# Kernel tuning notes

Measured on AMD Instinct MI355X. Metric: run time of the kernel, lower is better.

Reference implementation:

```python
import jax, jax.numpy as jnp
import numpy as np

N_NODES = 50000
N_EDGES = 400000
IN_DIM = 256
EPS_BN = 1e-5


def _bn(x, gamma, beta):
    # BatchNorm over nodes (training-mode batch statistics)
    m = jnp.mean(x, axis=0)
    v = jnp.var(x, axis=0)
    return (x - m) * jax.lax.rsqrt(v + EPS_BN) * gamma + beta


def _gcn(x, W, b, src, dst, n):
    # PyG GCNConv: add self-loops, symmetric deg^-1/2 normalization
    h = x @ W  # [N, F_out]
    deg = jax.ops.segment_sum(jnp.ones_like(dst, dtype=h.dtype), dst, num_segments=n) + 1.0
    dinv = jax.lax.rsqrt(deg)
    coef = dinv[src] * dinv[dst]  # [E]
    agg = jax.ops.segment_sum(h[src] * coef[:, None], dst, num_segments=n)
    agg = agg + h * (dinv * dinv)[:, None]  # self-loop contribution
    return agg + b


def _gat(x, W, a_src, a_dst, b, src, dst, n):
    # PyG GATConv, heads=H, concat=False (mean over heads)
    H, F = a_src.shape
    h = (x @ W).reshape(n, H, F)
    asc = jnp.einsum('nhf,hf->nh', h, a_src)
    adc = jnp.einsum('nhf,hf->nh', h, a_dst)
    loops = jnp.arange(n, dtype=src.dtype)
    s = jnp.concatenate([src, loops])
    d = jnp.concatenate([dst, loops])
    e = jax.nn.leaky_relu(asc[s] + adc[d], 0.2)  # [E+N, H]
    mx = jax.ops.segment_max(e, d, num_segments=n)
    ee = jnp.exp(e - mx[d])
    denom = jax.ops.segment_sum(ee, d, num_segments=n)
    alpha = ee / (denom[d] + 1e-16)  # edge softmax over incoming edges
    out = jax.ops.segment_sum(alpha[:, :, None] * h[s], d, num_segments=n)  # [N,H,F]
    return out.mean(axis=1) + b


def setup_inputs() -> dict:
    key = jax.random.key(0)
    ks = jax.random.split(key, 24)

    def glorot(k, shape):
        fan = shape[0] + shape[-1]
        return jax.random.normal(k, shape, jnp.float32) * np.sqrt(2.0 / fan)

    d = {}
    d['x'] = jax.random.normal(ks[0], (N_NODES, IN_DIM), jnp.float32)
    d['edge_index'] = jax.random.randint(ks[1], (2, N_EDGES), 0, N_NODES, jnp.int32)
    # GCNConv 1: 256 -> 256
    d['w1'] = glorot(ks[2], (IN_DIM, 256)); d['b1'] = jnp.zeros((256,), jnp.float32)
    d['g1'] = jnp.ones((256,), jnp.float32); d['be1'] = jnp.zeros((256,), jnp.float32)
    # GATConv: 256 -> 128, heads=4, concat=False
    d['gat_w'] = glorot(ks[3], (256, 4 * 128))
    d['gat_as'] = glorot(ks[4], (4, 128))
    d['gat_ad'] = glorot(ks[5], (4, 128))
    d['gat_b'] = jnp.zeros((128,), jnp.float32)
    d['g2'] = jnp.ones((128,), jnp.float32); d['be2'] = jnp.zeros((128,), jnp.float32)
    # GCNConv 3..5
    d['w3'] = glorot(ks[6], (128, 64)); d['b3'] = jnp.zeros((64,), jnp.float32)
    d['g3'] = jnp.ones((64,), jnp.float32); d['be3'] = jnp.zeros((64,), jnp.float32)
    d['w4'] = glorot(ks[7], (64, 32)); d['b4'] = jnp.zeros((32,), jnp.float32)
    d['g4'] = jnp.ones((32,), jnp.float32); d['be4'] = jnp.zeros((32,), jnp.float32)
    d['w5'] = glorot(ks[8], (32, 16)); d['b5'] = jnp.zeros((16,), jnp.float32)
    d['g5'] = jnp.ones((16,), jnp.float32); d['be5'] = jnp.zeros((16,), jnp.float32)
    # FC head
    d['fw1'] = glorot(ks[9], (16, 8)); d['fb1'] = jnp.zeros((8,), jnp.float32)
    d['fw2'] = glorot(ks[10], (8, 3)); d['fb2'] = jnp.zeros((3,), jnp.float32)
    return d


def reference(x, edge_index, w1, b1, g1, be1, gat_w, gat_as, gat_ad, gat_b, g2, be2,
              w3, b3, g3, be3, w4, b4, g4, be4, w5, b5, g5, be5, fw1, fb1, fw2, fb2):
    n = x.shape[0]
    src, dst = edge_index[0], edge_index[1]
    lrelu = lambda h: jax.nn.leaky_relu(h, 0.01)
    # dropout is identity in eval mode
    h = lrelu(_bn(_gcn(x, w1, b1, src, dst, n), g1, be1))
    h = lrelu(_bn(_gat(h, gat_w, gat_as, gat_ad, gat_b, src, dst, n), g2, be2))
    h = lrelu(_bn(_gcn(h, w3, b3, src, dst, n), g3, be3))
    h = lrelu(_bn(_gcn(h, w4, b4, src, dst, n), g4, be4))
    h = lrelu(_bn(_gcn(h, w5, b5, src, dst, n), g5, be5))
    h = lrelu(h @ fw1 + fb1)
    h = h @ fw2 + fb2
    return jax.nn.log_softmax(h, axis=1)
```

## Files before the change

kernel.cpp:

```cpp
#include <hip/hip_runtime.h>

#define NN 50000
#define NE 400000
#define GSTAT 2048

typedef short bf16x8 __attribute__((ext_vector_type(8)));
typedef float f32x4 __attribute__((ext_vector_type(4)));

__device__ __forceinline__ float lrelu01(float v) { return v >= 0.f ? v : 0.01f * v; }
__device__ __forceinline__ float lrelu02(float v) { return v >= 0.f ? v : 0.2f * v; }

__device__ __forceinline__ ushort f2bf(float f) {
  union { float f; unsigned u; } v; v.f = f;
  unsigned u = v.u;
  return (ushort)((u + 0x7FFFu + ((u >> 16) & 1u)) >> 16);
}
__device__ __forceinline__ float bf2f(ushort u) {
  union { unsigned u; float f; } v; v.u = ((unsigned)u) << 16;
  return v.f;
}

__global__ void wprep(const float* __restrict__ w1, const float* __restrict__ gw,
                      const float* __restrict__ w3, const float* __restrict__ w4,
                      const float* __restrict__ w5,
                      ushort* __restrict__ w1T, ushort* __restrict__ gwT,
                      ushort* __restrict__ w3T, ushort* __restrict__ w4T,
                      ushort* __restrict__ w5T) {
  int i = blockIdx.x * 256 + threadIdx.x;
  const float* W; ushort* WT; int K, N, j;
  if (i < 65536)        { W = w1; WT = w1T; K = 256; N = 256; j = i; }
  else if (i < 196608)  { W = gw; WT = gwT; K = 256; N = 512; j = i - 65536; }
  else if (i < 204800)  { W = w3; WT = w3T; K = 128; N = 64;  j = i - 196608; }
  else if (i < 206848)  { W = w4; WT = w4T; K = 64;  N = 32;  j = i - 204800; }
  else if (i < 207360)  { W = w5; WT = w5T; K = 32;  N = 16;  j = i - 206848; }
  else return;
  int k = j / N, c = j % N;
  WT[(size_t)c * K + k] = f2bf(W[(size_t)j]);
}

__global__ void count_kernel(const int* __restrict__ dst, int* __restrict__ counts, int e) {
  int i = blockIdx.x * 256 + threadIdx.x;
  if (i < e) atomicAdd(&counts[dst[i]], 1);
}

__global__ __launch_bounds__(256) void block_count_sum(const int* __restrict__ counts,
                                                       int* __restrict__ bsum,
                                                       float* __restrict__ dinv, int n) {
  int i = blockIdx.x * 256 + threadIdx.x;
  int c = (i < n) ? counts[i] : 0;
  if (i < n) dinv[i] = rsqrtf((float)c + 1.0f);
  int s = c;
#pragma unroll
  for (int off = 32; off > 0; off >>= 1) s += __shfl_down(s, off);
  __shared__ int ws[4];
  if ((threadIdx.x & 63) == 0) ws[threadIdx.x >> 6] = s;
  __syncthreads();
  if (threadIdx.x == 0) bsum[blockIdx.x] = ws[0] + ws[1] + ws[2] + ws[3];
}

__global__ __launch_bounds__(256) void scan_bsum(int* __restrict__ bsum, int nb) {
  __shared__ int sh[256];
  int v = (threadIdx.x < nb) ? bsum[threadIdx.x] : 0;
  sh[threadIdx.x] = v;
  __syncthreads();
  for (int off = 1; off < 256; off <<= 1) {
    int t = (threadIdx.x >= off) ? sh[threadIdx.x - off] : 0;
    __syncthreads();
    sh[threadIdx.x] += t;
    __syncthreads();
  }
  if (threadIdx.x < nb) bsum[threadIdx.x] = sh[threadIdx.x] - v;
}

__global__ __launch_bounds__(256) void row_start_kernel(const int* __restrict__ counts,
                                                        const int* __restrict__ bsum,
                                                        int* __restrict__ row_start, int n) {
  __shared__ int sh[256];
  int i = blockIdx.x * 256 + threadIdx.x;
  int c = (i < n) ? counts[i] : 0;
  sh[threadIdx.x] = c;
  __syncthreads();
  for (int off = 1; off < 256; off <<= 1) {
    int t = (threadIdx.x >= off) ? sh[threadIdx.x - off] : 0;
    __syncthreads();
    sh[threadIdx.x] += t;
    __syncthreads();
  }
  int incl = sh[threadIdx.x];
  int base = bsum[blockIdx.x];
  if (i < n) row_start[i] = base + incl - c;
  if (i == n - 1) row_start[n] = base + incl;
}

__global__ void fill_kernel(const int* __restrict__ src, const int* __restrict__ dst,
                            const int* __restrict__ row_start, int* __restrict__ cursor,
                            int* __restrict__ csr, int e) {
  int i = blockIdx.x * 256 + threadIdx.x;
  if (i >= e) return;
  int d = dst[i];
  int pos = atomicAdd(&cursor[d], 1);
  csr[row_start[d] + pos] = src[i];
}

__global__ __launch_bounds__(256) void gemm_mfma_x(const float* __restrict__ A,
                                                   const ushort* __restrict__ BT,
                                                   ushort* __restrict__ C,
                                                   int M, int K, int N,
                                                   const float* __restrict__ rowscale) {
  __shared__ ushort As[128][40];
  __shared__ ushort Bs[128][40];
  const int tid = threadIdx.x;
  const int bm = blockIdx.x * 128;
  const int bn = blockIdx.y * 128;
  const int wave = tid >> 6, lane = tid & 63;
  const int wr = (wave >> 1) * 64;
  const int wc = (wave & 1) * 64;
  const int lr = lane & 15;
  const int lk = (lane >> 4) * 8;

  f32x4 acc[4][4];
#pragma unroll
  for (int m = 0; m < 4; ++m)
#pragma unroll
    for (int n = 0; n < 4; ++n)
#pragma unroll
      for (int q = 0; q < 4; ++q) acc[m][n][q] = 0.f;

  for (int k0 = 0; k0 < K; k0 += 32) {
#pragma unroll
    for (int it = 0; it < 2; ++it) {
      int s = tid + it * 256;
      int r = s >> 2;
      int c = (s & 3) * 8;
      int grow = bm + r; if (grow >= M) grow = M - 1;
      float4 va = *reinterpret_cast<const float4*>(&A[(size_t)grow * K + k0 + c]);
      float4 vb = *reinterpret_cast<const float4*>(&A[(size_t)grow * K + k0 + c + 4]);
      ushort4 lo = make_ushort4(f2bf(va.x), f2bf(va.y), f2bf(va.z), f2bf(va.w));
      ushort4 hi = make_ushort4(f2bf(vb.x), f2bf(vb.y), f2bf(vb.z), f2bf(vb.w));
      *reinterpret_cast<ushort4*>(&As[r][c]) = lo;
      *reinterpret_cast<ushort4*>(&As[r][c + 4]) = hi;
    }
#pragma unroll
    for (int it = 0; it < 2; ++it) {
      int s = tid + it * 256;
      int r = s >> 2;
      int c = (s & 3) * 8;
      int4 v = *reinterpret_cast<const int4*>(&BT[(size_t)(bn + r) * K + k0 + c]);
      *reinterpret_cast<int4*>(&Bs[r][c]) = v;
    }
    __syncthreads();

    bf16x8 af[4], bfr[4];
#pragma unroll
    for (int m = 0; m < 4; ++m)
      af[m] = *reinterpret_cast<const bf16x8*>(&As[wr + m * 16 + lr][lk]);
#pragma unroll
    for (int n = 0; n < 4; ++n)
      bfr[n] = *reinterpret_cast<const bf16x8*>(&Bs[wc + n * 16 + lr][lk]);
#pragma unroll
    for (int m = 0; m < 4; ++m)
#pragma unroll
      for (int n = 0; n < 4; ++n)
        acc[m][n] = __builtin_amdgcn_mfma_f32_16x16x32_bf16(af[m], bfr[n], acc[m][n], 0, 0, 0);
    __syncthreads();
  }

  const int rbase = (lane >> 4) * 4;
  const int cbase = lane & 15;
#pragma unroll
  for (int m = 0; m < 4; ++m) {
#pragma unroll
    for (int q = 0; q < 4; ++q) {
      int row = bm + wr + m * 16 + rbase + q;
      if (row >= M) continue;
      float sc = rowscale ? rowscale[row] : 1.f;
#pragma unroll
      for (int n = 0; n < 4; ++n) {
        int col = bn + wc + n * 16 + cbase;
        C[(size_t)row * N + col] = f2bf(acc[m][n][q] * sc);
      }
    }
  }
}

__global__ __launch_bounds__(256) void gemm_mfma_bn(const ushort* __restrict__ A,
                                                    const ushort* __restrict__ BT,
                                                    ushort* __restrict__ C,
                                                    int M, int K, int N,
                                                    const float* __restrict__ rowscale,
                                                    const float* __restrict__ stats,
                                                    const float* __restrict__ gamma,
                                                    const float* __restrict__ beta) {
  __shared__ ushort As[128][40];
  __shared__ ushort Bs[128][40];
  __shared__ float scl[256], shl[256];
  const int tid = threadIdx.x;
  const float inv_n = 1.0f / (float)NN;
  for (int k = tid; k < K; k += 256) {
    float mean = stats[k] * inv_n;
    float var = stats[K + k] * inv_n - mean * mean;
    float sc = gamma[k] * rsqrtf(var + 1e-5f);
    scl[k] = sc;
    shl[k] = beta[k] - mean * sc;
  }
  const int bm = blockIdx.x * 128;
  const int bn = blockIdx.y * 128;
  const int wave = tid >> 6, lane = tid & 63;
  const int wr = (wave >> 1) * 64;
  const int wc = (wave & 1) * 64;
  const int lr = lane & 15;
  const int lk = (lane >> 4) * 8;

  f32x4 acc[4][4];
#pragma unroll
  for (int m = 0; m < 4; ++m)
#pragma unroll
    for (int n = 0; n < 4; ++n)
#pragma unroll
      for (int q = 0; q < 4; ++q) acc[m][n][q] = 0.f;
  __syncthreads();

  for (int k0 = 0; k0 < K; k0 += 32) {
#pragma unroll
    for (int it = 0; it < 2; ++it) {
      int s = tid + it * 256;
      int r = s >> 2;
      int c = (s & 3) * 8;
      int grow = bm + r; if (grow >= M) grow = M - 1;
      int4 v = *reinterpret_cast<const int4*>(&A[(size_t)grow * K + k0 + c]);
      ushort* u = reinterpret_cast<ushort*>(&v);
      ushort tmp[8];
#pragma unroll
      for (int j = 0; j < 8; ++j) {
        float f = bf2f(u[j]) * scl[k0 + c + j] + shl[k0 + c + j];
        tmp[j] = f2bf(f >= 0.f ? f : 0.01f * f);
      }
      *reinterpret_cast<int4*>(&As[r][c]) = *reinterpret_cast<int4*>(tmp);
    }
#pragma unroll
    for (int it = 0; it < 2; ++it) {
      int s = tid + it * 256;
      int r = s >> 2;
      int c = (s & 3) * 8;
      int4 v = *reinterpret_cast<const int4*>(&BT[(size_t)(bn + r) * K + k0 + c]);
      *reinterpret_cast<int4*>(&Bs[r][c]) = v;
    }
    __syncthreads();

    bf16x8 af[4], bfr[4];
#pragma unroll
    for (int m = 0; m < 4; ++m)
      af[m] = *reinterpret_cast<const bf16x8*>(&As[wr + m * 16 + lr][lk]);
#pragma unroll
    for (int n = 0; n < 4; ++n)
      bfr[n] = *reinterpret_cast<const bf16x8*>(&Bs[wc + n * 16 + lr][lk]);
#pragma unroll
    for (int m = 0; m < 4; ++m)
#pragma unroll
      for (int n = 0; n < 4; ++n)
        acc[m][n] = __builtin_amdgcn_mfma_f32_16x16x32_bf16(af[m], bfr[n], acc[m][n], 0, 0, 0);
    __syncthreads();
  }

  const int rbase = (lane >> 4) * 4;
  const int cbase = lane & 15;
#pragma unroll
  for (int m = 0; m < 4; ++m) {
#pragma unroll
    for (int q = 0; q < 4; ++q) {
      int row = bm + wr + m * 16 + rbase + q;
      if (row >= M) continue;
      float sc = rowscale ? rowscale[row] : 1.f;
#pragma unroll
      for (int n = 0; n < 4; ++n) {
        int col = bn + wc + n * 16 + cbase;
        C[(size_t)row * N + col] = f2bf(acc[m][n][q] * sc);
      }
    }
  }
}

template <int TN>
__global__ __launch_bounds__(256) void gemm_mfma_n_bn(const ushort* __restrict__ A,
                                                      const ushort* __restrict__ BT,
                                                      ushort* __restrict__ C,
                                                      int M, int K,
                                                      const float* __restrict__ rowscale,
                                                      const float* __restrict__ stats,
                                                      const float* __restrict__ gamma,
                                                      const float* __restrict__ beta) {
  __shared__ ushort As[128][40];
  __shared__ ushort Bs[TN][40];
  __shared__ float scl[128], shl[128];
  const int tid = threadIdx.x;
  const float inv_n = 1.0f / (float)NN;
  if (tid < K) {
    float mean = stats[tid] * inv_n;
    float var = stats[K + tid] * inv_n - mean * mean;
    float sc = gamma[tid] * rsqrtf(var + 1e-5f);
    scl[tid] = sc;
    shl[tid] = beta[tid] - mean * sc;
  }
  const int bm = blockIdx.x * 128;
  const int wave = tid >> 6, lane = tid & 63;
  const int wr = wave * 32;
  const int lr = lane & 15;
  const int lk = (lane >> 4) * 8;
  constexpr int NF = TN / 16;

  f32x4 acc[2][NF];
#pragma unroll
  for (int m = 0; m < 2; ++m)
#pragma unroll
    for (int n = 0; n < NF; ++n)
#pragma unroll
      for (int q = 0; q < 4; ++q) acc[m][n][q] = 0.f;
  __syncthreads();

  for (int k0 = 0; k0 < K; k0 += 32) {
#pragma unroll
    for (int it = 0; it < 2; ++it) {
      int s = tid + it * 256;
      int r = s >> 2;
      int c = (s & 3) * 8;
      int grow = bm + r; if (grow >= M) grow = M - 1;
      int4 v = *reinterpret_cast<const int4*>(&A[(size_t)grow * K + k0 + c]);
      ushort* u = reinterpret_cast<ushort*>(&v);
      ushort tmp[8];
#pragma unroll
      for (int j = 0; j < 8; ++j) {
        float f = bf2f(u[j]) * scl[k0 + c + j] + shl[k0 + c + j];
        tmp[j] = f2bf(f >= 0.f ? f : 0.01f * f);
      }
      *reinterpret_cast<int4*>(&As[r][c]) = *reinterpret_cast<int4*>(tmp);
    }
    if (tid < TN * 4) {
      int r = tid >> 2;
      int c = (tid & 3) * 8;
      int4 v = *reinterpret_cast<const int4*>(&BT[(size_t)r * K + k0 + c]);
      *reinterpret_cast<int4*>(&Bs[r][c]) = v;
    }
    __syncthreads();

    bf16x8 af[2], bfr[NF];
#pragma unroll
    for (int m = 0; m < 2; ++m)
      af[m] = *reinterpret_cast<const bf16x8*>(&As[wr + m * 16 + lr][lk]);
#pragma unroll
    for (int n = 0; n < NF; ++n)
      bfr[n] = *reinterpret_cast<const bf16x8*>(&Bs[n * 16 + lr][lk]);
#pragma unroll
    for (int m = 0; m < 2; ++m)
#pragma unroll
      for (int n = 0; n < NF; ++n)
        acc[m][n] = __builtin_amdgcn_mfma_f32_16x16x32_bf16(af[m], bfr[n], acc[m][n], 0, 0, 0);
    __syncthreads();
  }

  const int rbase = (lane >> 4) * 4;
  const int cbase = lane & 15;
#pragma unroll
  for (int m = 0; m < 2; ++m) {
#pragma unroll
    for (int q = 0; q < 4; ++q) {
      int row = bm + wr + m * 16 + rbase + q;
      if (row >= M) continue;
      float sc = rowscale ? rowscale[row] : 1.f;
#pragma unroll
      for (int n = 0; n < NF; ++n) {
        int col = n * 16 + cbase;
        C[(size_t)row * TN + col] = f2bf(acc[m][n][q] * sc);
      }
    }
  }
}

template <int F>
__global__ __launch_bounds__(256) void gcn_agg_stats(const ushort* __restrict__ h,
                                                     const int* __restrict__ row_start,
                                                     const int* __restrict__ csr,
                                                     const float* __restrict__ dinv,
                                                     ushort* __restrict__ out,
                                                     float* __restrict__ partials, int n) {
  constexpr int LPN = F / 8;
  constexpr int NPB = 256 / LPN;
  const int tid = threadIdx.x;
  const int sub = tid / LPN;
  const int f8 = (tid % LPN) * 8;
  float ps[8], pq[8];
#pragma unroll
  for (int j = 0; j < 8; ++j) { ps[j] = 0.f; pq[j] = 0.f; }

  for (int node = blockIdx.x * NPB + sub; node < n; node += GSTAT * NPB) {
    float di = dinv[node];
    float a[8];
    {
      int4 v = *reinterpret_cast<const int4*>(&h[(size_t)node * F + f8]);
      const ushort* u = reinterpret_cast<const ushort*>(&v);
#pragma unroll
      for (int j = 0; j < 8; ++j) a[j] = bf2f(u[j]);
    }
    int s0 = row_start[node], s1 = row_start[node + 1];
    int e = s0;
    for (; e + 3 < s1; e += 4) {
      int sA = csr[e], sB = csr[e + 1], sC = csr[e + 2], sD = csr[e + 3];
      int4 vA = *reinterpret_cast<const int4*>(&h[(size_t)sA * F + f8]);
      int4 vB = *reinterpret_cast<const int4*>(&h[(size_t)sB * F + f8]);
      int4 vC = *reinterpret_cast<const int4*>(&h[(size_t)sC * F + f8]);
      int4 vD = *reinterpret_cast<const int4*>(&h[(size_t)sD * F + f8]);
      const ushort* uA = reinterpret_cast<const ushort*>(&vA);
      const ushort* uB = reinterpret_cast<const ushort*>(&vB);
      const ushort* uC = reinterpret_cast<const ushort*>(&vC);
      const ushort* uD = reinterpret_cast<const ushort*>(&vD);
#pragma unroll
      for (int j = 0; j < 8; ++j)
        a[j] += (bf2f(uA[j]) + bf2f(uB[j])) + (bf2f(uC[j]) + bf2f(uD[j]));
    }
    for (; e < s1; ++e) {
      int sA = csr[e];
      int4 vA = *reinterpret_cast<const int4*>(&h[(size_t)sA * F + f8]);
      const ushort* uA = reinterpret_cast<const ushort*>(&vA);
#pragma unroll
      for (int j = 0; j < 8; ++j) a[j] += bf2f(uA[j]);
    }
    ushort u[8];
#pragma unroll
    for (int j = 0; j < 8; ++j) {
      a[j] *= di;
      u[j] = f2bf(a[j]);
      ps[j] += a[j];
      pq[j] += a[j] * a[j];
    }
    *reinterpret_cast<int4*>(&out[(size_t)node * F + f8]) = *reinterpret_cast<int4*>(u);
  }

  __shared__ float red[NPB][2 * F];
#pragma unroll
  for (int j = 0; j < 8; ++j) {
    red[sub][f8 + j] = ps[j];
    red[sub][F + f8 + j] = pq[j];
  }
  __syncthreads();
  for (int c = tid; c < 2 * F; c += 256) {
    float t = 0.f;
#pragma unroll 4
    for (int s = 0; s < NPB; ++s) t += red[s][c];
    partials[(size_t)c * GSTAT + blockIdx.x] = t;
  }
}

__global__ __launch_bounds__(256) void gat_softmax_norm(const int* __restrict__ row_start,
                                                        const int* __restrict__ csr,
                                                        const float* __restrict__ asc,
                                                        const float* __restrict__ adc,
                                                        float* __restrict__ alpha,
                                                        float* __restrict__ wnorm, int n) {
  int i = blockIdx.x * 256 + threadIdx.x;
  if (i >= 4 * n) return;
  int node = i >> 2, h = i & 3;
  int s0 = row_start[node], s1 = row_start[node + 1];
  float ad = adc[i];
  float eself = lrelu02(asc[i] + ad);
  float m = eself;
  for (int e = s0; e < s1; ++e) {
    float v = lrelu02(asc[csr[e] * 4 + h] + ad);
    alpha[(size_t)e * 4 + h] = v;
    m = fmaxf(m, v);
  }
  float ws = __expf(eself - m);
  float den = ws;
  for (int e = s0; e < s1; ++e) {
    float w = __expf(alpha[(size_t)e * 4 + h] - m);
    alpha[(size_t)e * 4 + h] = w;
    den += w;
  }
  float coef = 0.25f / (den + 1e-16f);
  wnorm[i] = ws * coef;
  for (int e = s0; e < s1; ++e) alpha[(size_t)e * 4 + h] *= coef;
}

__global__ __launch_bounds__(256) void gat_agg_v3(const ushort* __restrict__ hg,
                                                  const int* __restrict__ row_start,
                                                  const int* __restrict__ csr,
                                                  const float* __restrict__ alpha,
                                                  const float* __restrict__ wnorm,
                                                  ushort* __restrict__ out,
                                                  float* __restrict__ partials, int n) {
  const int tid = threadIdx.x;
  const int wave = tid >> 6, lane = tid & 63;
  const int h = lane >> 4;
  const int l = lane & 15;
  const int f8 = l * 8;
  float ps[8], pq[8];
#pragma unroll
  for (int j = 0; j < 8; ++j) { ps[j] = 0.f; pq[j] = 0.f; }

  const ushort* base = hg + h * 128 + f8;
  for (int node = blockIdx.x * 4 + wave; node < n; node += GSTAT * 4) {
    float a[8];
    {
      float w = wnorm[node * 4 + h];
      int4 v = *reinterpret_cast<const int4*>(base + (size_t)node * 512);
      const ushort* u = reinterpret_cast<const ushort*>(&v);
#pragma unroll
      for (int j = 0; j < 8; ++j) a[j] = w * bf2f(u[j]);
    }
    int s0 = row_start[node], s1 = row_start[node + 1];
    int e = s0;
    for (; e + 3 < s1; e += 4) {
      int sA = csr[e], sB = csr[e + 1], sC = csr[e + 2], sD = csr[e + 3];
      float wA = alpha[(size_t)e * 4 + h];
      float wB = alpha[(size_t)(e + 1) * 4 + h];
      float wC = alpha[(size_t)(e + 2) * 4 + h];
      float wD = alpha[(size_t)(e + 3) * 4 + h];
      int4 vA = *reinterpret_cast<const int4*>(base + (size_t)sA * 512);
      int4 vB = *reinterpret_cast<const int4*>(base + (size_t)sB * 512);
      int4 vC = *reinterpret_cast<const int4*>(base + (size_t)sC * 512);
      int4 vD = *reinterpret_cast<const int4*>(base + (size_t)sD * 512);
      const ushort* uA = reinterpret_cast<const ushort*>(&vA);
      const ushort* uB = reinterpret_cast<const ushort*>(&vB);
      const ushort* uC = reinterpret_cast<const ushort*>(&vC);
      const ushort* uD = reinterpret_cast<const ushort*>(&vD);
#pragma unroll
      for (int j = 0; j < 8; ++j)
        a[j] += (wA * bf2f(uA[j]) + wB * bf2f(uB[j]))
              + (wC * bf2f(uC[j]) + wD * bf2f(uD[j]));
    }
    for (; e < s1; ++e) {
      int sA = csr[e];
      float wA = alpha[(size_t)e * 4 + h];
      int4 vA = *reinterpret_cast<const int4*>(base + (size_t)sA * 512);
      const ushort* uA = reinterpret_cast<const ushort*>(&vA);
#pragma unroll
      for (int j = 0; j < 8; ++j) a[j] += wA * bf2f(uA[j]);
    }
#pragma unroll
    for (int j = 0; j < 8; ++j) {
      a[j] += __shfl_xor(a[j], 16);
      a[j] += __shfl_xor(a[j], 32);
    }
    if (h == 0) {
      ushort u[8];
#pragma unroll
      for (int j = 0; j < 8; ++j) {
        u[j] = f2bf(a[j]);
        ps[j] += a[j];
        pq[j] += a[j] * a[j];
      }
      *reinterpret_cast<int4*>(&out[(size_t)node * 128 + f8]) = *reinterpret_cast<int4*>(u);
    }
  }

  __shared__ float red[4][256];
  if (h == 0) {
#pragma unroll
    for (int j = 0; j < 8; ++j) {
      red[wave][f8 + j] = ps[j];
      red[wave][128 + f8 + j] = pq[j];
    }
  }
  __syncthreads();
  {
    int c = tid;
    float t = red[0][c] + red[1][c] + red[2][c] + red[3][c];
    partials[(size_t)c * GSTAT + blockIdx.x] = t;
  }
}

__global__ __launch_bounds__(256) void bn_reduce_col(const float* __restrict__ partials,
                                                     float* __restrict__ stats) {
  int c = blockIdx.x;
  float s = 0.f;
  for (int b = threadIdx.x; b < GSTAT; b += 256) s += partials[(size_t)c * GSTAT + b];
#pragma unroll
  for (int off = 32; off > 0; off >>= 1) s += __shfl_down(s, off);
  __shared__ float ws[4];
  if ((threadIdx.x & 63) == 0) ws[threadIdx.x >> 6] = s;
  __syncthreads();
  if (threadIdx.x == 0) stats[c] = ws[0] + ws[1] + ws[2] + ws[3];
}

__global__ __launch_bounds__(256) void gat_scores_bf(const ushort* __restrict__ hg,
                                                     const float* __restrict__ a_src,
                                                     const float* __restrict__ a_dst,
                                                     float* __restrict__ asc,
                                                     float* __restrict__ adc, int n) {
  int node = blockIdx.x;
  int head = threadIdx.x >> 6;
  int lane = threadIdx.x & 63;
  ushort2 v = *reinterpret_cast<const ushort2*>(&hg[(size_t)node * 512 + head * 128 + lane * 2]);
  float v0 = bf2f(v.x), v1 = bf2f(v.y);
  float s = v0 * a_src[head * 128 + lane * 2] + v1 * a_src[head * 128 + lane * 2 + 1];
  float d = v0 * a_dst[head * 128 + lane * 2] + v1 * a_dst[head * 128 + lane * 2 + 1];
#pragma unroll
  for (int off = 32; off > 0; off >>= 1) {
    s += __shfl_down(s, off);
    d += __shfl_down(d, off);
  }
  if (lane == 0) {
    asc[node * 4 + head] = s;
    adc[node * 4 + head] = d;
  }
}

__global__ __launch_bounds__(256) void head_kernel_bn(const ushort* __restrict__ h,
                                                      const float* __restrict__ stats,
                                                      const float* __restrict__ g5,
                                                      const float* __restrict__ be5,
                                                      const float* __restrict__ fw1,
                                                      const float* __restrict__ fb1,
                                                      const float* __restrict__ fw2,
                                                      const float* __restrict__ fb2,
                                                      float* __restrict__ out, int n) {
  __shared__ float scl[16], shl[16];
  if (threadIdx.x < 16) {
    const float inv_n = 1.0f / (float)NN;
    int k = threadIdx.x;
    float mean = stats[k] * inv_n;
    float var = stats[16 + k] * inv_n - mean * mean;
    float sc = g5[k] * rsqrtf(var + 1e-5f);
    scl[k] = sc;
    shl[k] = be5[k] - mean * sc;
  }
  __syncthreads();
  int i = blockIdx.x * 256 + threadIdx.x;
  if (i >= n) return;
  int4 ra = *reinterpret_cast<const int4*>(&h[(size_t)i * 16]);
  int4 rb = *reinterpret_cast<const int4*>(&h[(size_t)i * 16 + 8]);
  ushort u[16];
  *reinterpret_cast<int4*>(&u[0]) = ra;
  *reinterpret_cast<int4*>(&u[8]) = rb;
  float xr[16];
#pragma unroll
  for (int k = 0; k < 16; ++k) {
    float v = bf2f(u[k]) * scl[k] + shl[k];
    xr[k] = v >= 0.f ? v : 0.01f * v;
  }
  float z[8];
#pragma unroll
  for (int j = 0; j < 8; ++j) z[j] = fb1[j];
#pragma unroll
  for (int k = 0; k < 16; ++k) {
    float a = xr[k];
#pragma unroll
    for (int j = 0; j < 8; ++j) z[j] += a * fw1[k * 8 + j];
  }
#pragma unroll
  for (int j = 0; j < 8; ++j) z[j] = lrelu01(z[j]);
  float l[3];
#pragma unroll
  for (int j = 0; j < 3; ++j) l[j] = fb2[j];
#pragma unroll
  for (int k = 0; k < 8; ++k) {
    float a = z[k];
#pragma unroll
    for (int j = 0; j < 3; ++j) l[j] += a * fw2[k * 3 + j];
  }
  float mx = fmaxf(l[0], fmaxf(l[1], l[2]));
  float se = __expf(l[0] - mx) + __expf(l[1] - mx) + __expf(l[2] - mx);
  float ls = __logf(se);
#pragma unroll
  for (int j = 0; j < 3; ++j) out[(size_t)i * 3 + j] = l[j] - mx - ls;
}

extern "C" void kernel_launch(void* const* d_in, const int* in_sizes, int n_in,
                              void* d_out, int out_size, void* d_ws, size_t ws_size,
                              hipStream_t stream) {
  const float* x      = (const float*)d_in[0];
  const int*   ei     = (const int*)d_in[1];
  const int*   srcI   = ei;
  const int*   dstI   = ei + NE;
  const float* w1     = (const float*)d_in[2];
  const float* g1     = (const float*)d_in[4];
  const float* be1    = (const float*)d_in[5];
  const float* gat_w  = (const float*)d_in[6];
  const float* gat_as = (const float*)d_in[7];
  const float* gat_ad = (const float*)d_in[8];
  const float* g2     = (const float*)d_in[10];
  const float* be2    = (const float*)d_in[11];
  const float* w3     = (const float*)d_in[12];
  const float* g3     = (const float*)d_in[14];
  const float* be3    = (const float*)d_in[15];
  const float* w4     = (const float*)d_in[16];
  const float* g4     = (const float*)d_in[18];
  const float* be4    = (const float*)d_in[19];
  const float* w5     = (const float*)d_in[20];
  const float* g5     = (const float*)d_in[22];
  const float* be5    = (const float*)d_in[23];
  const float* fw1    = (const float*)d_in[24];
  const float* fb1    = (const float*)d_in[25];
  const float* fw2    = (const float*)d_in[26];
  const float* fb2    = (const float*)d_in[27];
  float* out = (float*)d_out;

  char* wsp = (char*)d_ws;
  size_t off = 0;
  auto alloc = [&](size_t bytes) -> void* {
    void* p = wsp + off;
    off += (bytes + 255) & ~(size_t)255;
    return p;
  };
  ushort* hw_bf  = (ushort*)alloc((size_t)NN * 512 * 2);
  ushort* r1     = (ushort*)alloc((size_t)NN * 256 * 2);
  ushort* r2     = (ushort*)alloc((size_t)NN * 128 * 2);
  ushort* r3     = (ushort*)alloc((size_t)NN * 64 * 2);
  ushort* r4     = (ushort*)alloc((size_t)NN * 32 * 2);
  ushort* r5     = (ushort*)alloc((size_t)NN * 16 * 2);
  ushort* w1T    = (ushort*)alloc((size_t)256 * 256 * 2);
  ushort* gwT    = (ushort*)alloc((size_t)512 * 256 * 2);
  ushort* w3T    = (ushort*)alloc((size_t)64 * 128 * 2);
  ushort* w4T    = (ushort*)alloc((size_t)32 * 64 * 2);
  ushort* w5T    = (ushort*)alloc((size_t)16 * 32 * 2);
  float*  dinv   = (float*)alloc((size_t)NN * 4);
  int*    counts = (int*)alloc((size_t)NN * 4);
  int*    cursor = (int*)alloc((size_t)NN * 4);
  int*    rstart = (int*)alloc((size_t)(NN + 4) * 4);
  int*    bsum   = (int*)alloc((size_t)256 * 4);
  int*    csr    = (int*)alloc((size_t)NE * 4);
  float*  asc    = (float*)alloc((size_t)NN * 4 * 4);
  float*  adc    = (float*)alloc((size_t)NN * 4 * 4);
  float*  wnorm  = (float*)alloc((size_t)NN * 4 * 4);
  float*  alpha  = (float*)alloc((size_t)NE * 4 * 4);
  float*  stats  = (float*)alloc(2048);
  float*  partials = (float*)alloc((size_t)512 * GSTAT * 4);

  const int egrid = (NE + 255) / 256;
  const int ngrid = (NN + 255) / 256;
  const int mblocks = (NN + 127) / 128;

  hipMemsetAsync(counts, 0, (size_t)NN * 4, stream);
  hipMemsetAsync(cursor, 0, (size_t)NN * 4, stream);
  count_kernel<<<egrid, 256, 0, stream>>>(dstI, counts, NE);
  block_count_sum<<<ngrid, 256, 0, stream>>>(counts, bsum, dinv, NN);
  scan_bsum<<<1, 256, 0, stream>>>(bsum, ngrid);
  row_start_kernel<<<ngrid, 256, 0, stream>>>(counts, bsum, rstart, NN);
  fill_kernel<<<egrid, 256, 0, stream>>>(srcI, dstI, rstart, cursor, csr, NE);

  wprep<<<810, 256, 0, stream>>>(w1, gat_w, w3, w4, w5, w1T, gwT, w3T, w4T, w5T);

  gemm_mfma_x<<<dim3(mblocks, 2), 256, 0, stream>>>(x, w1T, hw_bf, NN, 256, 256, dinv);
  gcn_agg_stats<256><<<GSTAT, 256, 0, stream>>>(hw_bf, rstart, csr, dinv, r1, partials, NN);
  bn_reduce_col<<<512, 256, 0, stream>>>(partials, stats);

  gemm_mfma_bn<<<dim3(mblocks, 4), 256, 0, stream>>>(r1, gwT, hw_bf, NN, 256, 512, nullptr,
                                                     stats, g1, be1);
  gat_scores_bf<<<NN, 256, 0, stream>>>(hw_bf, gat_as, gat_ad, asc, adc, NN);
  gat_softmax_norm<<<(4 * NN + 255) / 256, 256, 0, stream>>>(rstart, csr, asc, adc, alpha, wnorm, NN);
  gat_agg_v3<<<GSTAT, 256, 0, stream>>>(hw_bf, rstart, csr, alpha, wnorm, r2, partials, NN);
  bn_reduce_col<<<256, 256, 0, stream>>>(partials, stats);

  gemm_mfma_n_bn<64><<<mblocks, 256, 0, stream>>>(r2, w3T, hw_bf, NN, 128, dinv, stats, g2, be2);
  gcn_agg_stats<64><<<GSTAT, 256, 0, stream>>>(hw_bf, rstart, csr, dinv, r3, partials, NN);
  bn_reduce_col<<<128, 256, 0, stream>>>(partials, stats);

  gemm_mfma_n_bn<32><<<mblocks, 256, 0, stream>>>(r3, w4T, hw_bf, NN, 64, dinv, stats, g3, be3);
  gcn_agg_stats<32><<<GSTAT, 256, 0, stream>>>(hw_bf, rstart, csr, dinv, r4, partials, NN);
  bn_reduce_col<<<64, 256, 0, stream>>>(partials, stats);

  gemm_mfma_n_bn<16><<<mblocks, 256, 0, stream>>>(r4, w5T, hw_bf, NN, 32, dinv, stats, g4, be4);
  gcn_agg_stats<16><<<GSTAT, 256, 0, stream>>>(hw_bf, rstart, csr, dinv, r5, partials, NN);
  bn_reduce_col<<<32, 256, 0, stream>>>(partials, stats);

  head_kernel_bn<<<ngrid, 256, 0, stream>>>(r5, stats, g5, be5, fw1, fb1, fw2, fb2, out, NN);
}
```

Before: 387.3 us.

## Fuse GAT attention scores into GEMM epilogue and defer softmax normalization

Computes the per-head source and destination attention scores inside the GAT projection GEMM epilogue, using shuffle reductions over each 128-column head tile, and removes the separate gat_scores_bf kernel that re-read the 50000x512 bf16 projection. The softmax kernel no longer makes a second pass to rescale alpha. It stores a per-node coefficient that the aggregation kernel applies once to its accumulator. The two memsets are also replaced with a single zeroing kernel. The cost is extra shared memory and shuffles in the GEMM epilogue, plus one extra coefficient buffer.

```diff
diff --git a/kernel.cpp b/kernel.cpp
--- a/kernel.cpp
+++ b/kernel.cpp
@@ -38,6 +38,11 @@
   WT[(size_t)c * K + k] = f2bf(W[(size_t)j]);
 }
 
+__global__ void zero2(int* __restrict__ a, int* __restrict__ b, int n) {
+  int i = blockIdx.x * 256 + threadIdx.x;
+  if (i < n) { a[i] = 0; b[i] = 0; }
+}
+
 __global__ void count_kernel(const int* __restrict__ dst, int* __restrict__ counts, int e) {
   int i = blockIdx.x * 256 + threadIdx.x;
   if (i < e) atomicAdd(&counts[dst[i]], 1);
@@ -187,13 +192,18 @@
                                                     const ushort* __restrict__ BT,
                                                     ushort* __restrict__ C,
                                                     int M, int K, int N,
-                                                    const float* __restrict__ rowscale,
                                                     const float* __restrict__ stats,
                                                     const float* __restrict__ gamma,
-                                                    const float* __restrict__ beta) {
+                                                    const float* __restrict__ beta,
+                                                    const float* __restrict__ a_srcg,
+                                                    const float* __restrict__ a_dstg,
+                                                    float* __restrict__ asc,
+                                                    float* __restrict__ adc) {
   __shared__ ushort As[128][40];
   __shared__ ushort Bs[128][40];
   __shared__ float scl[256], shl[256];
+  __shared__ float asrc[128], adst[128];
+  __shared__ float sred[128][2], dred[128][2];
   const int tid = threadIdx.x;
   const float inv_n = 1.0f / (float)NN;
   for (int k = tid; k < K; k += 256) {
@@ -203,6 +213,10 @@
     scl[k] = sc;
     shl[k] = beta[k] - mean * sc;
   }
+  if (tid < 128) {
+    asrc[tid] = a_srcg[blockIdx.y * 128 + tid];
+    adst[tid] = a_dstg[blockIdx.y * 128 + tid];
+  }
   const int bm = blockIdx.x * 128;
   const int bn = blockIdx.y * 128;
   const int wave = tid >> 6, lane = tid & 63;
@@ -268,14 +282,35 @@
   for (int m = 0; m < 4; ++m) {
 #pragma unroll
     for (int q = 0; q < 4; ++q) {
-      int row = bm + wr + m * 16 + rbase + q;
-      if (row >= M) continue;
-      float sc = rowscale ? rowscale[row] : 1.f;
+      int rloc = wr + m * 16 + rbase + q;
+      int row = bm + rloc;
+      float s = 0.f, d = 0.f;
 #pragma unroll
       for (int n = 0; n < 4; ++n) {
-        int col = bn + wc + n * 16 + cbase;
-        C[(size_t)row * N + col] = f2bf(acc[m][n][q] * sc);
+        int colin = wc + n * 16 + cbase;
+        ushort ub = f2bf(acc[m][n][q]);
+        float vv = bf2f(ub);
+        if (row < M) C[(size_t)row * N + bn + colin] = ub;
+        s += vv * asrc[colin];
+        d += vv * adst[colin];
       }
+#pragma unroll
+      for (int w = 1; w < 16; w <<= 1) {
+        s += __shfl_xor(s, w);
+        d += __shfl_xor(d, w);
+      }
+      if ((lane & 15) == 0) {
+        sred[rloc][wave & 1] = s;
+        dred[rloc][wave & 1] = d;
+      }
+    }
+  }
+  __syncthreads();
+  if (tid < 128) {
+    int grow = bm + tid;
+    if (grow < M) {
+      asc[(size_t)grow * 4 + blockIdx.y] = sred[tid][0] + sred[tid][1];
+      adc[(size_t)grow * 4 + blockIdx.y] = dred[tid][0] + dred[tid][1];
     }
   }
 }
@@ -454,7 +489,8 @@
                                                         const float* __restrict__ asc,
                                                         const float* __restrict__ adc,
                                                         float* __restrict__ alpha,
-                                                        float* __restrict__ wnorm, int n) {
+                                                        float* __restrict__ wnorm,
+                                                        float* __restrict__ coefs, int n) {
   int i = blockIdx.x * 256 + threadIdx.x;
   if (i >= 4 * n) return;
   int node = i >> 2, h = i & 3;
@@ -474,9 +510,8 @@
     alpha[(size_t)e * 4 + h] = w;
     den += w;
   }
-  float coef = 0.25f / (den + 1e-16f);
-  wnorm[i] = ws * coef;
-  for (int e = s0; e < s1; ++e) alpha[(size_t)e * 4 + h] *= coef;
+  wnorm[i] = ws;
+  coefs[i] = 0.25f / (den + 1e-16f);
 }
 
 __global__ __launch_bounds__(256) void gat_agg_v3(const ushort* __restrict__ hg,
@@ -484,6 +519,7 @@
                                                   const int* __restrict__ csr,
                                                   const float* __restrict__ alpha,
                                                   const float* __restrict__ wnorm,
+                                                  const float* __restrict__ coefs,
                                                   ushort* __restrict__ out,
                                                   float* __restrict__ partials, int n) {
   const int tid = threadIdx.x;
@@ -534,8 +570,10 @@
 #pragma unroll
       for (int j = 0; j < 8; ++j) a[j] += wA * bf2f(uA[j]);
     }
+    float cf = coefs[node * 4 + h];
 #pragma unroll
     for (int j = 0; j < 8; ++j) {
+      a[j] *= cf;
       a[j] += __shfl_xor(a[j], 16);
       a[j] += __shfl_xor(a[j], 32);
     }
@@ -578,29 +616,6 @@
   if ((threadIdx.x & 63) == 0) ws[threadIdx.x >> 6] = s;
   __syncthreads();
   if (threadIdx.x == 0) stats[c] = ws[0] + ws[1] + ws[2] + ws[3];
-}
-
-__global__ __launch_bounds__(256) void gat_scores_bf(const ushort* __restrict__ hg,
-                                                     const float* __restrict__ a_src,
-                                                     const float* __restrict__ a_dst,
-                                                     float* __restrict__ asc,
-                                                     float* __restrict__ adc, int n) {
-  int node = blockIdx.x;
-  int head = threadIdx.x >> 6;
-  int lane = threadIdx.x & 63;
-  ushort2 v = *reinterpret_cast<const ushort2*>(&hg[(size_t)node * 512 + head * 128 + lane * 2]);
-  float v0 = bf2f(v.x), v1 = bf2f(v.y);
-  float s = v0 * a_src[head * 128 + lane * 2] + v1 * a_src[head * 128 + lane * 2 + 1];
-  float d = v0 * a_dst[head * 128 + lane * 2] + v1 * a_dst[head * 128 + lane * 2 + 1];
-#pragma unroll
-  for (int off = 32; off > 0; off >>= 1) {
-    s += __shfl_down(s, off);
-    d += __shfl_down(d, off);
-  }
-  if (lane == 0) {
-    asc[node * 4 + head] = s;
-    adc[node * 4 + head] = d;
-  }
 }
 
 __global__ __launch_bounds__(256) void head_kernel_bn(const ushort* __restrict__ h,
@@ -720,6 +735,7 @@
   float*  asc    = (float*)alloc((size_t)NN * 4 * 4);
   float*  adc    = (float*)alloc((size_t)NN * 4 * 4);
   float*  wnorm  = (float*)alloc((size_t)NN * 4 * 4);
+  float*  coefs  = (float*)alloc((size_t)NN * 4 * 4);
   float*  alpha  = (float*)alloc((size_t)NE * 4 * 4);
   float*  stats  = (float*)alloc(2048);
   float*  partials = (float*)alloc((size_t)512 * GSTAT * 4);
@@ -728,8 +744,7 @@
   const int ngrid = (NN + 255) / 256;
   const int mblocks = (NN + 127) / 128;
 
-  hipMemsetAsync(counts, 0, (size_t)NN * 4, stream);
-  hipMemsetAsync(cursor, 0, (size_t)NN * 4, stream);
+  zero2<<<ngrid, 256, 0, stream>>>(counts, cursor, NN);
   count_kernel<<<egrid, 256, 0, stream>>>(dstI, counts, NE);
   block_count_sum<<<ngrid, 256, 0, stream>>>(counts, bsum, dinv, NN);
   scan_bsum<<<1, 256, 0, stream>>>(bsum, ngrid);
@@ -742,11 +757,11 @@
   gcn_agg_stats<256><<<GSTAT, 256, 0, stream>>>(hw_bf, rstart, csr, dinv, r1, partials, NN);
   bn_reduce_col<<<512, 256, 0, stream>>>(partials, stats);
 
-  gemm_mfma_bn<<<dim3(mblocks, 4), 256, 0, stream>>>(r1, gwT, hw_bf, NN, 256, 512, nullptr,
-                                                     stats, g1, be1);
-  gat_scores_bf<<<NN, 256, 0, stream>>>(hw_bf, gat_as, gat_ad, asc, adc, NN);
-  gat_softmax_norm<<<(4 * NN + 255) / 256, 256, 0, stream>>>(rstart, csr, asc, adc, alpha, wnorm, NN);
-  gat_agg_v3<<<GSTAT, 256, 0, stream>>>(hw_bf, rstart, csr, alpha, wnorm, r2, partials, NN);
+  gemm_mfma_bn<<<dim3(mblocks, 4), 256, 0, stream>>>(r1, gwT, hw_bf, NN, 256, 512,
+                                                     stats, g1, be1, gat_as, gat_ad, asc, adc);
+  gat_softmax_norm<<<(4 * NN + 255) / 256, 256, 0, stream>>>(rstart, csr, asc, adc, alpha,
+                                                             wnorm, coefs, NN);
+  gat_agg_v3<<<GSTAT, 256, 0, stream>>>(hw_bf, rstart, csr, alpha, wnorm, coefs, r2, partials, NN);
   bn_reduce_col<<<256, 256, 0, stream>>>(partials, stats);
 
   gemm_mfma_n_bn<64><<<mblocks, 256, 0, stream>>>(r2, w3T, hw_bf, NN, 128, dinv, stats, g2, be2);
```

New measurement: 361.0 us. 1.07x faster.
